# Performance work log

Hardware: AMD Instinct MI355X
Metric: run time of the kernel (lower is better)

Reference implementation:

```python
import jax, jax.numpy as jnp
import numpy as np

B, T, D, H, CL = 2, 4096, 2048, 16, 512
DK = D // H          # key_dim == head_dim (value_factor=1) == 128
SCALING = DK ** -0.5


def _rel_pos():
    # RetNet relative position: per-head decay gamma, rotary sin/cos, chunk decay masks
    h = np.arange(H, dtype=np.float64)
    gamma = 1.0 - 2.0 ** (-5.0 - h)                           # (H,)
    angle = 1.0 / (10000.0 ** (np.arange(0, DK, 2) / DK))
    angle = np.repeat(angle, 2)                               # (DK,) each freq duplicated
    pos = np.arange(T)[:, None] * angle[None, :]              # (T, DK)
    sin, cos = np.sin(pos), np.cos(pos)
    idx = np.arange(CL)
    expn = idx[:, None] - idx[None, :]                        # (CL, CL)
    m = np.where(expn >= 0, gamma[:, None, None] ** np.maximum(expn, 0), 0.0)  # (H,CL,CL)
    scale = np.sqrt(m.sum(-1, keepdims=True))                 # (H,CL,1)
    mask = m / scale
    cross_decay = (gamma ** CL)[:, None, None]                # (H,1,1)
    inner = gamma[:, None] ** (idx + 1)                       # (H,CL)
    inner_decay = inner[:, :, None] / (scale / mask[:, -1].sum(-1)[:, None, None])  # (H,CL,1)
    f32 = lambda a: jnp.asarray(a, jnp.float32)
    return f32(sin), f32(cos), f32(mask), f32(cross_decay), f32(inner_decay)


def setup_inputs() -> dict:
    key = jax.random.key(0)
    kx, kq, kk, kv, kg, ko = jax.random.split(key, 6)
    sin, cos, mask, cross_decay, inner_decay = _rel_pos()
    mk = lambda k: jax.random.normal(k, (D, D), jnp.float32) * 0.02  # ~xavier w/ small gain
    z = jnp.zeros((D,), jnp.float32)
    return dict(
        x=jax.random.normal(kx, (B, T, D), jnp.float32),
        sin=sin, cos=cos, mask=mask, cross_decay=cross_decay, inner_decay=inner_decay,
        wq=mk(kq), bq=z, wk=mk(kk), bk=z, wv=mk(kv), bv=z, wg=mk(kg), bg=z,
        wo=jax.random.normal(ko, (D, D), jnp.float32) * (1.0 / np.sqrt(D)), bo=z,
    )


def _rotate_every_two(x):
    x1, x2 = x[..., ::2], x[..., 1::2]
    return jnp.stack((-x2, x1), axis=-1).reshape(x.shape)


def _theta_shift(x, sin, cos):
    return x * cos + _rotate_every_two(x) * sin


def reference(x, sin, cos, mask, cross_decay, inner_decay,
              wq, bq, wk, bk, wv, bv, wg, bg, wo, bo):
    NC = T // CL
    q = (x @ wq.T + bq).reshape(B, T, H, DK).transpose(0, 2, 1, 3)           # (B,H,T,DK)
    k = ((x @ wk.T + bk) * SCALING).reshape(B, T, H, DK).transpose(0, 2, 1, 3)
    v = x @ wv.T + bv                                                        # (B,T,D)
    g = x @ wg.T + bg
    qr = _theta_shift(q, sin, cos)
    kr = _theta_shift(k, sin, cos)
    # chunk views -> (B, NC, H, CL, DK)
    qr = qr.reshape(B, H, NC, CL, DK).transpose(0, 2, 1, 3, 4)
    kr = kr.reshape(B, H, NC, CL, DK).transpose(0, 2, 1, 3, 4)
    vc = v.reshape(B, NC, CL, H, DK).transpose(0, 1, 3, 2, 4)                # (B,NC,H,CL,HD)
    # intra-chunk decay-masked attention
    qk = jnp.einsum('bnhld,bnhmd->bnhlm', qr, kr) * mask                      # (B,NC,H,CL,CL)
    inner_scale = jnp.clip(jnp.abs(jax.lax.stop_gradient(qk)).sum(-1, keepdims=True), 1.0)
    inner_out = jnp.einsum('bnhlm,bnhmd->bnhld', qk / inner_scale, vc)
    # per-chunk KV contribution (keys weighted by remaining decay = last mask row)
    kv = jnp.einsum('bnhlk,bnhld->bnhkd', kr, vc * mask[:, -1, :, None])      # (B,NC,H,DK,HD)

    def step(carry, kv_i):
        kv_state, kv_scale = carry
        out = (kv_state / kv_scale, kv_scale)
        new_state = kv_state * cross_decay + kv_i
        s = jnp.abs(jax.lax.stop_gradient(new_state)).sum(-2, keepdims=True)
        new_scale = jnp.clip(s.max(-1, keepdims=True), 1.0)
        return (new_state, new_scale), out

    init = (jnp.zeros((B, H, DK, DK), x.dtype), jnp.ones((B, H, 1, 1), x.dtype))
    _, (kv_rec, cross_scale) = jax.lax.scan(step, init, jnp.moveaxis(kv, 1, 0))
    kv_rec = jnp.moveaxis(kv_rec, 0, 1)            # (B,NC,H,DK,HD)
    cross_scale = jnp.moveaxis(cross_scale, 0, 1)  # (B,NC,H,1,1)
    all_scale = jnp.maximum(inner_scale, cross_scale)
    cross_out = jnp.einsum('bnhlk,bnhkd->bnhld', qr * inner_decay, kv_rec)
    out = inner_out / (all_scale / inner_scale) + cross_out / (all_scale / cross_scale)
    out = out.transpose(0, 1, 3, 2, 4)             # (B,NC,CL,H,HD)
    # group_norm: LayerNorm over head_dim, no affine, eps=1e-6
    mu = out.mean(-1, keepdims=True)
    var = ((out - mu) ** 2).mean(-1, keepdims=True)
    out = (out - mu) / jnp.sqrt(var + 1e-6)
    out = out.reshape(B, T, D)
    out = jax.nn.silu(g) * out                     # swish gate
    return out @ wo.T + bo
```

## Files before the change

### kernel.cpp

```cpp
#include <hip/hip_runtime.h>
#include <hip/hip_bf16.h>
#include <math.h>

#define NB   2
#define NT   4096
#define ND   2048
#define NH   16
#define NDK  128
#define NCL  512
#define NNC  8
#define NTOK 8192
#define SCALING 0.08838834764831845f

typedef unsigned short u16;
typedef short short8 __attribute__((ext_vector_type(8)));
typedef unsigned short ushort8 __attribute__((ext_vector_type(8)));
typedef float f32x4 __attribute__((ext_vector_type(4)));
typedef float float4v __attribute__((ext_vector_type(4)));
typedef short short4v __attribute__((ext_vector_type(4)));

__device__ __forceinline__ float bf2f(u16 u) {
    union { unsigned int i; float f; } v; v.i = ((unsigned int)u) << 16; return v.f;
}
__device__ __forceinline__ u16 f2bf(float f) {
    union { float f; unsigned int i; } v; v.f = f;
    unsigned int r = v.i + 0x7FFFu + ((v.i >> 16) & 1u);
    return (u16)(r >> 16);
}

__device__ __forceinline__ void gload16(const void* g, void* l) {
    __builtin_amdgcn_global_load_lds(
        (const __attribute__((address_space(1))) unsigned int*)g,
        (__attribute__((address_space(3))) unsigned int*)l, 16, 0, 0);
}

__device__ __forceinline__ void gemm_bt_core(
    const u16* __restrict__ A, const u16* __restrict__ Bm,
    int lda, int ldb, int K, u16* As, u16* Bs, f32x4 acc[4][4])
{
    const int tid  = threadIdx.x;
    const int lane = tid & 63;
    const int lr   = lane & 15;
    const int lg   = lane >> 4;
    const int wid  = tid >> 6;
    const int wr   = (wid >> 1) * 64;
    const int wc   = (wid & 1) * 64;
    for (int kt = 0; kt < K; kt += 64) {
#pragma unroll
        for (int i = 0; i < 4; ++i) {
            int c = tid + i * 256;
            int row = c >> 3, col = (c & 7) * 8;
            gload16(A  + (size_t)row * lda + kt + col, (char*)As + (size_t)c * 16);
            gload16(Bm + (size_t)row * ldb + kt + col, (char*)Bs + (size_t)c * 16);
        }
        __syncthreads();
#pragma unroll
        for (int kk = 0; kk < 2; ++kk) {
            short8 a[4], b[4];
#pragma unroll
            for (int m = 0; m < 4; ++m)
                a[m] = *(const short8*)(As + (wr + m * 16 + lr) * 64 + kk * 32 + lg * 8);
#pragma unroll
            for (int n = 0; n < 4; ++n)
                b[n] = *(const short8*)(Bs + (wc + n * 16 + lr) * 64 + kk * 32 + lg * 8);
#pragma unroll
            for (int m = 0; m < 4; ++m)
#pragma unroll
                for (int n = 0; n < 4; ++n)
                    acc[m][n] = __builtin_amdgcn_mfma_f32_16x16x32_bf16(a[m], b[n], acc[m][n], 0, 0, 0);
        }
        __syncthreads();
    }
}

__global__ __launch_bounds__(256) void k_f2bf(const float* __restrict__ src,
                                              u16* __restrict__ dst, int n4)
{
    int i = blockIdx.x * blockDim.x + threadIdx.x;
    int stride = gridDim.x * blockDim.x;
    for (int j = i; j < n4; j += stride) {
        float4v f = *(const float4v*)(src + (size_t)j * 4);
        short4v o;
        o.x = (short)f2bf(f.x); o.y = (short)f2bf(f.y);
        o.z = (short)f2bf(f.z); o.w = (short)f2bf(f.w);
        *(short4v*)(dst + (size_t)j * 4) = o;
    }
}

__global__ __launch_bounds__(256) void k_gemm1(
    const u16* __restrict__ xb, const u16* __restrict__ wb,
    const float* __restrict__ bq, const float* __restrict__ bk,
    const float* __restrict__ bv, const float* __restrict__ bg,
    const float* __restrict__ sinp, const float* __restrict__ cosp,
    const float* __restrict__ maskp,
    u16* __restrict__ qro, u16* __restrict__ kro, u16* __restrict__ krwT,
    u16* __restrict__ vT, u16* __restrict__ glin)
{
    __shared__ __align__(16) u16 As[128 * 64];
    __shared__ __align__(16) u16 Bs[128 * 64];
    f32x4 acc[4][4];
#pragma unroll
    for (int m = 0; m < 4; ++m)
#pragma unroll
        for (int n = 0; n < 4; ++n) acc[m][n] = (f32x4){0.f, 0.f, 0.f, 0.f};

    int mt = blockIdx.x, nt = blockIdx.y;
    gemm_bt_core(xb + (size_t)mt * 128 * ND, wb + (size_t)nt * 128 * ND, ND, ND, ND, As, Bs, acc);

    int tid = threadIdx.x, lane = tid & 63, lr = lane & 15, lg = lane >> 4, wid = tid >> 6;
    int wr = (wid >> 1) * 64, wc = (wid & 1) * 64;
    int which = nt >> 4;

    if (which <= 1) {
        const float* bias = (which == 0) ? bq : bk;
#pragma unroll
        for (int m = 0; m < 4; ++m) {
#pragma unroll
            for (int n = 0; n < 4; ++n) {
#pragma unroll
                for (int r = 0; r < 4; ++r) {
                    int row = mt * 128 + wr + m * 16 + lg * 4 + r;
                    int col = nt * 128 + wc + n * 16 + lr;
                    int f = col & 2047, h = f >> 7, d = f & 127;
                    int b = row >> 12, t = row & 4095, cn = t >> 9, cl = t & 511;
                    float v = acc[m][n][r] + bias[f];
                    if (which == 1) v *= SCALING;
                    float sv = sinp[(size_t)t * NDK + d];
                    float cv = cosp[(size_t)t * NDK + d];
                    float vp = __shfl_xor(v, 1);
                    float rot = (lr & 1) ? vp : -vp;
                    float o = v * cv + rot * sv;
                    size_t chbase = (size_t)(b * NNC + cn) * NH + h;
                    if (which == 0) {
                        qro[(chbase * NCL + cl) * NDK + d] = f2bf(o);
                    } else {
                        kro[(chbase * NCL + cl) * NDK + d] = f2bf(o);
                        float w = maskp[((size_t)h * NCL + (NCL - 1)) * NCL + cl];
                        krwT[(chbase * NDK + d) * NCL + cl] = f2bf(o * w);
                    }
                }
            }
        }
    } else {
#pragma unroll
        for (int m = 0; m < 4; ++m) {
#pragma unroll
            for (int n = 0; n < 4; ++n) {
#pragma unroll
                for (int r = 0; r < 4; ++r) {
                    int row = mt * 128 + wr + m * 16 + lg * 4 + r;
                    int col = nt * 128 + wc + n * 16 + lr;
                    int f = col & 2047;
                    float v = acc[m][n][r];
                    if (which == 2) {
                        int h = f >> 7, d = f & 127;
                        int b = row >> 12, t = row & 4095, cn = t >> 9, cl = t & 511;
                        vT[(((size_t)(b * NNC + cn) * NH + h) * NDK + d) * NCL + cl] = f2bf(v + bv[f]);
                    } else {
                        glin[(size_t)row * ND + f] = f2bf(v + bg[f]);
                    }
                }
            }
        }
    }
}

__global__ __launch_bounds__(256) void k_gemm2(
    const u16* __restrict__ y, const u16* __restrict__ wob,
    const float* __restrict__ bo, float* __restrict__ out)
{
    __shared__ __align__(16) u16 As[128 * 64];
    __shared__ __align__(16) u16 Bs[128 * 64];
    f32x4 acc[4][4];
#pragma unroll
    for (int m = 0; m < 4; ++m)
#pragma unroll
        for (int n = 0; n < 4; ++n) acc[m][n] = (f32x4){0.f, 0.f, 0.f, 0.f};

    int mt = blockIdx.y, nt = blockIdx.x;
    gemm_bt_core(y + (size_t)mt * 128 * ND, wob + (size_t)nt * 128 * ND, ND, ND, ND, As, Bs, acc);

    int tid = threadIdx.x, lane = tid & 63, lr = lane & 15, lg = lane >> 4, wid = tid >> 6;
    int wr = (wid >> 1) * 64, wc = (wid & 1) * 64;
#pragma unroll
    for (int m = 0; m < 4; ++m)
#pragma unroll
        for (int n = 0; n < 4; ++n)
#pragma unroll
            for (int r = 0; r < 4; ++r) {
                int row = mt * 128 + wr + m * 16 + lg * 4 + r;
                int col = nt * 128 + wc + n * 16 + lr;
                out[(size_t)row * ND + col] = acc[m][n][r] + bo[col];
            }
}

__global__ __launch_bounds__(256) void k_inner(
    const u16* __restrict__ qr, const u16* __restrict__ kr,
    const u16* __restrict__ vT, const float* __restrict__ mask,
    float* __restrict__ iraw, float* __restrict__ iscale)
{
    __shared__ __align__(16) u16 Qs[128 * 128];
    __shared__ __align__(16) u16 Ks[32 * 128];
    __shared__ __align__(16) u16 Vs[128 * 32];
    __shared__ __align__(16) u16 Ps[4][32 * 32];
    __shared__ float sl[128];

    int qt = blockIdx.x, bnh = blockIdx.y;
    int h = bnh & 15;
    const u16* Q = qr + (size_t)bnh * NCL * NDK + (size_t)qt * 128 * NDK;
    const u16* K = kr + (size_t)bnh * NCL * NDK;
    const u16* V = vT + (size_t)bnh * NDK * NCL;
    const float* M = mask + (size_t)h * NCL * NCL + (size_t)qt * 128 * NCL;

    int tid = threadIdx.x, lane = tid & 63, lr = lane & 15, lg = lane >> 4, wid = tid >> 6;
    if (tid < 128) sl[tid] = 0.f;
#pragma unroll
    for (int i = 0; i < 8; ++i) {
        int c = tid + i * 256;
        gload16(Q + (size_t)c * 8, (char*)Qs + (size_t)c * 16);
    }
    __syncthreads();

    short8 aq[2][4];
#pragma unroll
    for (int i = 0; i < 2; ++i)
#pragma unroll
        for (int kk = 0; kk < 4; ++kk)
            aq[i][kk] = *(const short8*)(Qs + (wid * 32 + i * 16 + lr) * 128 + kk * 32 + lg * 8);

    f32x4 acc[2][8];
#pragma unroll
    for (int i = 0; i < 2; ++i)
#pragma unroll
        for (int n = 0; n < 8; ++n) acc[i][n] = (f32x4){0.f, 0.f, 0.f, 0.f};

    int msteps = qt * 4 + 4;
    for (int ms = 0; ms < msteps; ++ms) {
        int mb = ms * 32;
#pragma unroll
        for (int i = 0; i < 2; ++i) {
            int c = tid + i * 256;
            int row = c >> 4, cc = (c & 15) * 8;
            gload16(K + (size_t)(mb + row) * NDK + cc, (char*)Ks + (size_t)c * 16);
        }
#pragma unroll
        for (int i = 0; i < 2; ++i) {
            int c = tid + i * 256;
            int row = c >> 2, cc = (c & 3) * 8;
            gload16(V + (size_t)row * NCL + mb + cc, (char*)Vs + (size_t)c * 16);
        }
        __syncthreads();

        f32x4 pa[2][2];
#pragma unroll
        for (int i = 0; i < 2; ++i) { pa[i][0] = (f32x4){0.f,0.f,0.f,0.f}; pa[i][1] = (f32x4){0.f,0.f,0.f,0.f}; }
#pragma unroll
        for (int kk = 0; kk < 4; ++kk) {
            short8 bk0 = *(const short8*)(Ks + (lr) * 128 + kk * 32 + lg * 8);
            short8 bk1 = *(const short8*)(Ks + (16 + lr) * 128 + kk * 32 + lg * 8);
#pragma unroll
            for (int i = 0; i < 2; ++i) {
                pa[i][0] = __builtin_amdgcn_mfma_f32_16x16x32_bf16(aq[i][kk], bk0, pa[i][0], 0, 0, 0);
                pa[i][1] = __builtin_amdgcn_mfma_f32_16x16x32_bf16(aq[i][kk], bk1, pa[i][1], 0, 0, 0);
            }
        }
#pragma unroll
        for (int i = 0; i < 2; ++i) {
#pragma unroll
            for (int r = 0; r < 4; ++r) {
                int rloc = i * 16 + lg * 4 + r;
                int row128 = wid * 32 + rloc;
                float m0 = M[(size_t)row128 * NCL + mb + lr];
                float m1 = M[(size_t)row128 * NCL + mb + 16 + lr];
                float p0 = pa[i][0][r] * m0;
                float p1 = pa[i][1][r] * m1;
                float ss = fabsf(p0) + fabsf(p1);
                ss += __shfl_xor(ss, 1); ss += __shfl_xor(ss, 2);
                ss += __shfl_xor(ss, 4); ss += __shfl_xor(ss, 8);
                if (lr == 0) sl[row128] += ss;
                Ps[wid][rloc * 32 + lr]      = f2bf(p0);
                Ps[wid][rloc * 32 + 16 + lr] = f2bf(p1);
            }
        }
        __syncthreads();

        short8 ap[2];
#pragma unroll
        for (int i = 0; i < 2; ++i)
            ap[i] = *(const short8*)(Ps[wid] + (i * 16 + lr) * 32 + lg * 8);
#pragma unroll
        for (int n = 0; n < 8; ++n) {
            short8 bv8 = *(const short8*)(Vs + (n * 16 + lr) * 32 + lg * 8);
#pragma unroll
            for (int i = 0; i < 2; ++i)
                acc[i][n] = __builtin_amdgcn_mfma_f32_16x16x32_bf16(ap[i], bv8, acc[i][n], 0, 0, 0);
        }
        __syncthreads();
    }

    float* OR = iraw + ((size_t)bnh * NCL + (size_t)qt * 128) * NDK;
#pragma unroll
    for (int i = 0; i < 2; ++i)
#pragma unroll
        for (int n = 0; n < 8; ++n)
#pragma unroll
            for (int r = 0; r < 4; ++r) {
                int row = wid * 32 + i * 16 + lg * 4 + r;
                int col = n * 16 + lr;
                OR[(size_t)row * NDK + col] = acc[i][n][r];
            }
    __syncthreads();
    if (tid < 128) iscale[(size_t)bnh * NCL + qt * 128 + tid] = fmaxf(1.f, sl[tid]);
}

__global__ __launch_bounds__(256) void k_kv(
    const u16* __restrict__ krwT, const u16* __restrict__ vT, float* __restrict__ kvi)
{
    __shared__ __align__(16) u16 As[128 * 64];
    __shared__ __align__(16) u16 Bs[128 * 64];
    f32x4 acc[4][4];
#pragma unroll
    for (int m = 0; m < 4; ++m)
#pragma unroll
        for (int n = 0; n < 4; ++n) acc[m][n] = (f32x4){0.f, 0.f, 0.f, 0.f};

    int bnh = blockIdx.x;
    gemm_bt_core(krwT + (size_t)bnh * NDK * NCL, vT + (size_t)bnh * NDK * NCL,
                 NCL, NCL, NCL, As, Bs, acc);

    int tid = threadIdx.x, lane = tid & 63, lr = lane & 15, lg = lane >> 4, wid = tid >> 6;
    int wr = (wid >> 1) * 64, wc = (wid & 1) * 64;
    float* O = kvi + (size_t)bnh * NDK * NDK;
#pragma unroll
    for (int m = 0; m < 4; ++m)
#pragma unroll
        for (int n = 0; n < 4; ++n)
#pragma unroll
            for (int r = 0; r < 4; ++r) {
                int row = wr + m * 16 + lg * 4 + r;
                int col = wc + n * 16 + lr;
                O[(size_t)row * NDK + col] = acc[m][n][r];
            }
}

__global__ __launch_bounds__(256) void k_scan(
    const float* __restrict__ kvi, const float* __restrict__ cdec,
    u16* __restrict__ kvrT, float* __restrict__ csc)
{
    int bh = blockIdx.x;
    int b = bh >> 4, h = bh & 15;
    float cd = cdec[h];
    int tid = threadIdx.x;
    int col = tid & 127;
    int r0 = (tid >> 7) * 64;
    float st[64];
#pragma unroll
    for (int i = 0; i < 64; ++i) st[i] = 0.f;
    float scale = 1.f;
    __shared__ float cs[128];
    __shared__ float scsh;

    for (int n = 0; n < NNC; ++n) {
        size_t idx = (size_t)((b * NNC + n) * NH + h);
        size_t kb = idx * (NDK * NDK);
        float inv = 1.f / scale;
#pragma unroll
        for (int i = 0; i < 64; ++i)
            kvrT[kb + (size_t)col * NDK + r0 + i] = f2bf(st[i] * inv);
        if (tid == 0) csc[idx] = scale;

        const float* KV = kvi + kb;
        float colsum = 0.f;
#pragma unroll
        for (int i = 0; i < 64; ++i) {
            float xv = st[i] * cd + KV[(size_t)(r0 + i) * NDK + col];
            st[i] = xv;
            colsum += fabsf(xv);
        }
        __syncthreads();
        if (tid < 128) cs[tid] = 0.f;
        __syncthreads();
        atomicAdd(&cs[col], colsum);
        __syncthreads();
        if (tid == 0) {
            float mx = cs[0];
            for (int i = 1; i < 128; ++i) mx = fmaxf(mx, cs[i]);
            scsh = fmaxf(1.f, mx);
        }
        __syncthreads();
        scale = scsh;
    }
}

__global__ __launch_bounds__(256) void k_combine(
    const u16* __restrict__ qr, const u16* __restrict__ kvrT,
    const float* __restrict__ iraw, const float* __restrict__ iscale,
    const float* __restrict__ cscale, const float* __restrict__ idecay,
    const u16* __restrict__ glin, u16* __restrict__ y)
{
    __shared__ __align__(16) u16 As[128 * 64];
    __shared__ __align__(16) u16 Bs[128 * 64];
    __shared__ float ssum[128];
    __shared__ float ssq[128];
    f32x4 acc[4][4];
#pragma unroll
    for (int m = 0; m < 4; ++m)
#pragma unroll
        for (int n = 0; n < 4; ++n) acc[m][n] = (f32x4){0.f, 0.f, 0.f, 0.f};

    int qt = blockIdx.x, bnh = blockIdx.y;
    int b = bnh >> 7, cn = (bnh >> 4) & 7, h = bnh & 15;
    gemm_bt_core(qr + (size_t)bnh * NCL * NDK + (size_t)qt * 128 * NDK,
                 kvrT + (size_t)bnh * NDK * NDK, NDK, NDK, NDK, As, Bs, acc);

    int tid = threadIdx.x, lane = tid & 63, lr = lane & 15, lg = lane >> 4, wid = tid >> 6;
    int wr = (wid >> 1) * 64, wc = (wid & 1) * 64;
    if (tid < 128) { ssum[tid] = 0.f; ssq[tid] = 0.f; }
    __syncthreads();
    float csv = cscale[bnh];

#pragma unroll
    for (int m = 0; m < 4; ++m) {
#pragma unroll
        for (int r = 0; r < 4; ++r) {
            int rloc = wr + m * 16 + lg * 4 + r;
            int l = qt * 128 + rloc;
            float isc = iscale[(size_t)bnh * NCL + l];
            float all = fmaxf(isc, csv);
            float c1 = 1.f / all;
            float c2 = (csv / all) * idecay[h * NCL + l];
            const float* ir = iraw + ((size_t)bnh * NCL + l) * NDK;
            float lsum = 0.f, lsq = 0.f;
#pragma unroll
            for (int n = 0; n < 4; ++n) {
                int col = wc + n * 16 + lr;
                float v = ir[col] * c1 + acc[m][n][r] * c2;
                acc[m][n][r] = v;
                lsum += v; lsq += v * v;
            }
            lsum += __shfl_xor(lsum, 1); lsum += __shfl_xor(lsum, 2);
            lsum += __shfl_xor(lsum, 4); lsum += __shfl_xor(lsum, 8);
            lsq  += __shfl_xor(lsq, 1);  lsq  += __shfl_xor(lsq, 2);
            lsq  += __shfl_xor(lsq, 4);  lsq  += __shfl_xor(lsq, 8);
            if (lr == 0) { atomicAdd(&ssum[rloc], lsum); atomicAdd(&ssq[rloc], lsq); }
        }
    }
    __syncthreads();
#pragma unroll
    for (int m = 0; m < 4; ++m) {
#pragma unroll
        for (int r = 0; r < 4; ++r) {
            int rloc = wr + m * 16 + lg * 4 + r;
            int l = qt * 128 + rloc;
            float mu = ssum[rloc] * (1.f / 128.f);
            float var = ssq[rloc] * (1.f / 128.f) - mu * mu;
            float rstd = rsqrtf(fmaxf(var, 0.f) + 1e-6f);
            int t = cn * NCL + l;
            size_t obase = ((size_t)(b * NT + t)) * ND + (size_t)h * NDK;
#pragma unroll
            for (int n = 0; n < 4; ++n) {
                int col = wc + n * 16 + lr;
                float gv = bf2f(glin[obase + col]);
                float sg = gv / (1.f + expf(-gv));
                float ov = (acc[m][n][r] - mu) * rstd * sg;
                y[obase + col] = f2bf(ov);
            }
        }
    }
}

extern "C" void kernel_launch(void* const* d_in, const int* in_sizes, int n_in,
                              void* d_out, int out_size, void* d_ws, size_t ws_size,
                              hipStream_t stream)
{
    const float* x    = (const float*)d_in[0];
    const float* sinp = (const float*)d_in[1];
    const float* cosp = (const float*)d_in[2];
    const float* mask = (const float*)d_in[3];
    const float* cdec = (const float*)d_in[4];
    const float* idec = (const float*)d_in[5];
    const float* wq   = (const float*)d_in[6];
    const float* bq   = (const float*)d_in[7];
    const float* wk   = (const float*)d_in[8];
    const float* bk   = (const float*)d_in[9];
    const float* wv   = (const float*)d_in[10];
    const float* bv   = (const float*)d_in[11];
    const float* wg   = (const float*)d_in[12];
    const float* bg   = (const float*)d_in[13];
    const float* wo   = (const float*)d_in[14];
    const float* bo   = (const float*)d_in[15];
    float* out = (float*)d_out;

    char* ws = (char*)d_ws;
    u16*   XB   = (u16*)(ws + 0);
    u16*   WB   = (u16*)(ws + 33554432);
    u16*   WOB  = (u16*)(ws + 67108864);
    u16*   QR   = (u16*)(ws + 75497472);
    u16*   KR   = (u16*)(ws + 109051904);
    u16*   KRWT = (u16*)(ws + 142606336);
    u16*   VT   = (u16*)(ws + 176160768);
    u16*   GLIN = (u16*)(ws + 209715200);
    float* KVI  = (float*)(ws + 243269632);
    float* CSC  = (float*)(ws + 260046848);
    float* IRAW = (float*)(ws + 0);
    u16*   Y    = KR;
    u16*   KVRT = KRWT;
    float* ISC  = (float*)(ws + 243269632);

    k_f2bf<<<2048, 256, 0, stream>>>(x, XB, 4194304);
    k_f2bf<<<1024, 256, 0, stream>>>(wq, WB,            1048576);
    k_f2bf<<<1024, 256, 0, stream>>>(wk, WB + 4194304,  1048576);
    k_f2bf<<<1024, 256, 0, stream>>>(wv, WB + 8388608,  1048576);
    k_f2bf<<<1024, 256, 0, stream>>>(wg, WB + 12582912, 1048576);
    k_f2bf<<<1024, 256, 0, stream>>>(wo, WOB,           1048576);

    k_gemm1<<<dim3(64, 64), 256, 0, stream>>>(XB, WB, bq, bk, bv, bg, sinp, cosp, mask,
                                              QR, KR, KRWT, VT, GLIN);
    k_kv<<<256, 256, 0, stream>>>(KRWT, VT, KVI);
    k_scan<<<32, 256, 0, stream>>>(KVI, cdec, KVRT, CSC);
    k_inner<<<dim3(4, 256), 256, 0, stream>>>(QR, KR, VT, mask, IRAW, ISC);
    k_combine<<<dim3(4, 256), 256, 0, stream>>>(QR, KVRT, IRAW, ISC, CSC, idec, GLIN, Y);
    k_gemm2<<<dim3(16, 64), 256, 0, stream>>>(Y, WOB, bo, out);
}
```

Before: 1.010 ms.

## Replace projection GEMMs with 256x256-tile double-buffered 8-wave MFMA core

```diff
diff --git a/kernel.cpp b/kernel.cpp
--- a/kernel.cpp
+++ b/kernel.cpp
@@ -34,6 +34,145 @@
         (__attribute__((address_space(3))) unsigned int*)l, 16, 0, 0);
 }
 
+#define MFMA16(acc_, a_, b_) acc_ = __builtin_amdgcn_mfma_f32_16x16x32_bf16(a_, b_, acc_, 0, 0, 0)
+#define SBAR  asm volatile("s_barrier" ::: "memory")
+
+
+__device__ __forceinline__ void stage_half(const u16* __restrict__ g, int ld,
+                                           u16* lds, int tid)
+{
+#pragma unroll
+    for (int j = 0; j < 2; ++j) {
+        int c = tid + j * 512;
+        int row = c >> 3, u = c & 7;
+        gload16(g + (size_t)row * ld + ((u ^ (row & 7)) * 8), lds + (size_t)c * 8);
+    }
+}
+
+__device__ __forceinline__ void gemm256_core(
+    const u16* __restrict__ Aop, const u16* __restrict__ Bop,
+    int lda, int ldb, int nkt, u16* Ab, u16* Bb, f32x4 acc[8][4])
+{
+    const int tid  = threadIdx.x;
+    const int lane = tid & 63;
+    const int lr   = lane & 15;
+    const int lg   = lane >> 4;
+    const int wid  = tid >> 6;
+    const int wm   = wid >> 2;
+    const int wn   = wid & 3;
+
+    u16* Abuf[2] = { Ab, Ab + 16384 };
+    u16* Bbuf[2] = { Bb, Bb + 16384 };
+
+    const int swz  = lr & 7;
+    const int uc0  = ((0 * 4 + lg) ^ swz) * 8;
+    const int uc1  = ((1 * 4 + lg) ^ swz) * 8;
+    const int arow = wm * 128 + lr;
+    const int brow = wn * 64 + lr;
+
+    stage_half(Bop,                       ldb, Bbuf[0],        tid);
+    stage_half(Bop + (size_t)128 * ldb,   ldb, Bbuf[0] + 8192, tid);
+    stage_half(Aop,                       lda, Abuf[0],        tid);
+    stage_half(Aop + (size_t)128 * lda,   lda, Abuf[0] + 8192, tid);
+    if (nkt > 1) {
+        stage_half(Bop + 64,                     ldb, Bbuf[1],        tid);
+        stage_half(Bop + (size_t)128 * ldb + 64, ldb, Bbuf[1] + 8192, tid);
+        stage_half(Aop + 64,                     lda, Abuf[1],        tid);
+        asm volatile("s_waitcnt vmcnt(6)" ::: "memory");
+    } else {
+        asm volatile("s_waitcnt vmcnt(0)" ::: "memory");
+    }
+    SBAR;
+
+    short8 a[4][2], bA[2][2], bB[2][2];
+
+    for (int G = 0; G < nkt; ++G) {
+        const u16* At = Abuf[G & 1];
+        const u16* Bt = Bbuf[G & 1];
+
+#pragma unroll
+        for (int mf = 0; mf < 4; ++mf) {
+            a[mf][0] = *(const short8*)(At + (size_t)(arow + mf * 16) * 64 + uc0);
+            a[mf][1] = *(const short8*)(At + (size_t)(arow + mf * 16) * 64 + uc1);
+        }
+#pragma unroll
+        for (int nf = 0; nf < 2; ++nf) {
+            bA[nf][0] = *(const short8*)(Bt + (size_t)(brow + nf * 16) * 64 + uc0);
+            bA[nf][1] = *(const short8*)(Bt + (size_t)(brow + nf * 16) * 64 + uc1);
+        }
+        if (G + 1 < nkt)
+            stage_half(Aop + (size_t)128 * lda + (size_t)(G + 1) * 64, lda,
+                       Abuf[(G + 1) & 1] + 8192, tid);
+        SBAR;
+        __builtin_amdgcn_s_setprio(1);
+#pragma unroll
+        for (int mf = 0; mf < 4; ++mf)
+#pragma unroll
+            for (int nf = 0; nf < 2; ++nf) {
+                MFMA16(acc[mf][nf], a[mf][0], bA[nf][0]);
+                MFMA16(acc[mf][nf], a[mf][1], bA[nf][1]);
+            }
+        __builtin_amdgcn_s_setprio(0);
+        SBAR;
+
+#pragma unroll
+        for (int nf = 0; nf < 2; ++nf) {
+            bB[nf][0] = *(const short8*)(Bt + (size_t)(brow + 32 + nf * 16) * 64 + uc0);
+            bB[nf][1] = *(const short8*)(Bt + (size_t)(brow + 32 + nf * 16) * 64 + uc1);
+        }
+        SBAR;
+        __builtin_amdgcn_s_setprio(1);
+#pragma unroll
+        for (int mf = 0; mf < 4; ++mf)
+#pragma unroll
+            for (int nf = 0; nf < 2; ++nf) {
+                MFMA16(acc[mf][2 + nf], a[mf][0], bB[nf][0]);
+                MFMA16(acc[mf][2 + nf], a[mf][1], bB[nf][1]);
+            }
+        __builtin_amdgcn_s_setprio(0);
+        SBAR;
+
+#pragma unroll
+        for (int mf = 0; mf < 4; ++mf) {
+            a[mf][0] = *(const short8*)(At + (size_t)(arow + 64 + mf * 16) * 64 + uc0);
+            a[mf][1] = *(const short8*)(At + (size_t)(arow + 64 + mf * 16) * 64 + uc1);
+        }
+        if (G + 2 < nkt)
+            stage_half(Bop + (size_t)(G + 2) * 64, ldb, Bbuf[G & 1], tid);
+        SBAR;
+        __builtin_amdgcn_s_setprio(1);
+#pragma unroll
+        for (int mf = 0; mf < 4; ++mf)
+#pragma unroll
+            for (int nf = 0; nf < 2; ++nf) {
+                MFMA16(acc[4 + mf][2 + nf], a[mf][0], bB[nf][0]);
+                MFMA16(acc[4 + mf][2 + nf], a[mf][1], bB[nf][1]);
+            }
+        __builtin_amdgcn_s_setprio(0);
+        SBAR;
+
+        if (G + 2 < nkt) {
+            stage_half(Bop + (size_t)128 * ldb + (size_t)(G + 2) * 64, ldb,
+                       Bbuf[G & 1] + 8192, tid);
+            stage_half(Aop + (size_t)(G + 2) * 64, lda, Abuf[G & 1], tid);
+            asm volatile("s_waitcnt vmcnt(6)" ::: "memory");
+        } else if (G + 1 < nkt) {
+            asm volatile("s_waitcnt vmcnt(0)" ::: "memory");
+        }
+        SBAR;
+        __builtin_amdgcn_s_setprio(1);
+#pragma unroll
+        for (int mf = 0; mf < 4; ++mf)
+#pragma unroll
+            for (int nf = 0; nf < 2; ++nf) {
+                MFMA16(acc[4 + mf][nf], a[mf][0], bA[nf][0]);
+                MFMA16(acc[4 + mf][nf], a[mf][1], bA[nf][1]);
+            }
+        __builtin_amdgcn_s_setprio(0);
+        SBAR;
+    }
+}
+
 __device__ __forceinline__ void gemm_bt_core(
     const u16* __restrict__ A, const u16* __restrict__ Bm,
     int lda, int ldb, int K, u16* As, u16* Bs, f32x4 acc[4][4])
@@ -87,7 +226,7 @@
     }
 }
 
-__global__ __launch_bounds__(256) void k_gemm1(
+__global__ __launch_bounds__(512, 2) void k_gemm1(
     const u16* __restrict__ xb, const u16* __restrict__ wb,
     const float* __restrict__ bq, const float* __restrict__ bk,
     const float* __restrict__ bv, const float* __restrict__ bg,
@@ -96,34 +235,38 @@
     u16* __restrict__ qro, u16* __restrict__ kro, u16* __restrict__ krwT,
     u16* __restrict__ vT, u16* __restrict__ glin)
 {
-    __shared__ __align__(16) u16 As[128 * 64];
-    __shared__ __align__(16) u16 Bs[128 * 64];
-    f32x4 acc[4][4];
-#pragma unroll
-    for (int m = 0; m < 4; ++m)
+    __shared__ __align__(16) u16 Ab[2 * 256 * 64];
+    __shared__ __align__(16) u16 Bb[2 * 256 * 64];
+    f32x4 acc[8][4];
+#pragma unroll
+    for (int m = 0; m < 8; ++m)
 #pragma unroll
         for (int n = 0; n < 4; ++n) acc[m][n] = (f32x4){0.f, 0.f, 0.f, 0.f};
 
-    int mt = blockIdx.x, nt = blockIdx.y;
-    gemm_bt_core(xb + (size_t)mt * 128 * ND, wb + (size_t)nt * 128 * ND, ND, ND, ND, As, Bs, acc);
+    int bid = blockIdx.x;
+    int swzb = (bid & 7) * 128 + (bid >> 3);
+    int mt = swzb >> 5, nt = swzb & 31;
+
+    gemm256_core(xb + (size_t)mt * 256 * ND, wb + (size_t)nt * 256 * ND,
+                 ND, ND, ND / 64, Ab, Bb, acc);
 
     int tid = threadIdx.x, lane = tid & 63, lr = lane & 15, lg = lane >> 4, wid = tid >> 6;
-    int wr = (wid >> 1) * 64, wc = (wid & 1) * 64;
-    int which = nt >> 4;
+    int wm = wid >> 2, wn = wid & 3;
+    int which = nt >> 3;
 
     if (which <= 1) {
         const float* bias = (which == 0) ? bq : bk;
 #pragma unroll
-        for (int m = 0; m < 4; ++m) {
-#pragma unroll
-            for (int n = 0; n < 4; ++n) {
+        for (int mf = 0; mf < 8; ++mf) {
+#pragma unroll
+            for (int nf = 0; nf < 4; ++nf) {
 #pragma unroll
                 for (int r = 0; r < 4; ++r) {
-                    int row = mt * 128 + wr + m * 16 + lg * 4 + r;
-                    int col = nt * 128 + wc + n * 16 + lr;
+                    int row = mt * 256 + wm * 128 + mf * 16 + lg * 4 + r;
+                    int col = nt * 256 + wn * 64 + nf * 16 + lr;
                     int f = col & 2047, h = f >> 7, d = f & 127;
                     int b = row >> 12, t = row & 4095, cn = t >> 9, cl = t & 511;
-                    float v = acc[m][n][r] + bias[f];
+                    float v = acc[mf][nf][r] + bias[f];
                     if (which == 1) v *= SCALING;
                     float sv = sinp[(size_t)t * NDK + d];
                     float cv = cosp[(size_t)t * NDK + d];
@@ -143,15 +286,15 @@
         }
     } else {
 #pragma unroll
-        for (int m = 0; m < 4; ++m) {
-#pragma unroll
-            for (int n = 0; n < 4; ++n) {
+        for (int mf = 0; mf < 8; ++mf) {
+#pragma unroll
+            for (int nf = 0; nf < 4; ++nf) {
 #pragma unroll
                 for (int r = 0; r < 4; ++r) {
-                    int row = mt * 128 + wr + m * 16 + lg * 4 + r;
-                    int col = nt * 128 + wc + n * 16 + lr;
+                    int row = mt * 256 + wm * 128 + mf * 16 + lg * 4 + r;
+                    int col = nt * 256 + wn * 64 + nf * 16 + lr;
                     int f = col & 2047;
-                    float v = acc[m][n][r];
+                    float v = acc[mf][nf][r];
                     if (which == 2) {
                         int h = f >> 7, d = f & 127;
                         int b = row >> 12, t = row & 4095, cn = t >> 9, cl = t & 511;
@@ -165,32 +308,36 @@
     }
 }
 
-__global__ __launch_bounds__(256) void k_gemm2(
+__global__ __launch_bounds__(512, 2) void k_gemm2(
     const u16* __restrict__ y, const u16* __restrict__ wob,
     const float* __restrict__ bo, float* __restrict__ out)
 {
-    __shared__ __align__(16) u16 As[128 * 64];
-    __shared__ __align__(16) u16 Bs[128 * 64];
-    f32x4 acc[4][4];
-#pragma unroll
-    for (int m = 0; m < 4; ++m)
+    __shared__ __align__(16) u16 Ab[2 * 256 * 64];
+    __shared__ __align__(16) u16 Bb[2 * 256 * 64];
+    f32x4 acc[8][4];
+#pragma unroll
+    for (int m = 0; m < 8; ++m)
 #pragma unroll
         for (int n = 0; n < 4; ++n) acc[m][n] = (f32x4){0.f, 0.f, 0.f, 0.f};
 
-    int mt = blockIdx.y, nt = blockIdx.x;
-    gemm_bt_core(y + (size_t)mt * 128 * ND, wob + (size_t)nt * 128 * ND, ND, ND, ND, As, Bs, acc);
+    int bid = blockIdx.x;
+    int swzb = (bid & 7) * 32 + (bid >> 3);
+    int mt = swzb >> 3, nt = swzb & 7;
+
+    gemm256_core(y + (size_t)mt * 256 * ND, wob + (size_t)nt * 256 * ND,
+                 ND, ND, ND / 64, Ab, Bb, acc);
 
     int tid = threadIdx.x, lane = tid & 63, lr = lane & 15, lg = lane >> 4, wid = tid >> 6;
-    int wr = (wid >> 1) * 64, wc = (wid & 1) * 64;
-#pragma unroll
-    for (int m = 0; m < 4; ++m)
-#pragma unroll
-        for (int n = 0; n < 4; ++n)
+    int wm = wid >> 2, wn = wid & 3;
+#pragma unroll
+    for (int mf = 0; mf < 8; ++mf)
+#pragma unroll
+        for (int nf = 0; nf < 4; ++nf)
 #pragma unroll
             for (int r = 0; r < 4; ++r) {
-                int row = mt * 128 + wr + m * 16 + lg * 4 + r;
-                int col = nt * 128 + wc + n * 16 + lr;
-                out[(size_t)row * ND + col] = acc[m][n][r] + bo[col];
+                int row = mt * 256 + wm * 128 + mf * 16 + lg * 4 + r;
+                int col = nt * 256 + wn * 64 + nf * 16 + lr;
+                out[(size_t)row * ND + col] = acc[mf][nf][r] + bo[col];
             }
 }
 
@@ -514,11 +661,11 @@
     k_f2bf<<<1024, 256, 0, stream>>>(wg, WB + 12582912, 1048576);
     k_f2bf<<<1024, 256, 0, stream>>>(wo, WOB,           1048576);
 
-    k_gemm1<<<dim3(64, 64), 256, 0, stream>>>(XB, WB, bq, bk, bv, bg, sinp, cosp, mask,
-                                              QR, KR, KRWT, VT, GLIN);
+    k_gemm1<<<1024, 512, 0, stream>>>(XB, WB, bq, bk, bv, bg, sinp, cosp, mask,
+                                      QR, KR, KRWT, VT, GLIN);
     k_kv<<<256, 256, 0, stream>>>(KRWT, VT, KVI);
     k_scan<<<32, 256, 0, stream>>>(KVI, cdec, KVRT, CSC);
     k_inner<<<dim3(4, 256), 256, 0, stream>>>(QR, KR, VT, mask, IRAW, ISC);
     k_combine<<<dim3(4, 256), 256, 0, stream>>>(QR, KVRT, IRAW, ISC, CSC, idec, GLIN, Y);
-    k_gemm2<<<dim3(16, 64), 256, 0, stream>>>(Y, WOB, bo, out);
-}
+    k_gemm2<<<256, 512, 0, stream>>>(Y, WOB, bo, out);
+}
```

After: 1.100 ms. 8.9% more time.
